# Kernel tuning notes

Hardware: AMD Instinct MI355X
Metric: run time of the kernel (lower is better)

Reference implementation:

```python
import jax, jax.numpy as jnp
import numpy as np

E = 256      # emb_size
H = 100      # ff_sim hidden
B, TQ, TK = 16, 128, 128


def setup_inputs() -> dict:
    key = jax.random.key(0)
    ks = jax.random.split(key, 8)
    queries = jax.random.normal(ks[0], (B, TQ, E), dtype=jnp.float32)
    keys = jax.random.normal(ks[1], (B, TK, E), dtype=jnp.float32)
    query_masks = jnp.ones((B, TQ), dtype=jnp.float32)
    key_masks = jnp.ones((B, TK), dtype=jnp.float32)
    # xavier_uniform bounds: sqrt(6/(fan_in+fan_out))
    def xavier(k, shape):
        fan_out, fan_in = shape
        lim = np.sqrt(6.0 / (fan_in + fan_out))
        return jax.random.uniform(k, shape, jnp.float32, -lim, lim)
    W1 = xavier(ks[2], (H, 2 * E))          # linear_ff_sim[0].weight
    b1 = jnp.zeros((H,), dtype=jnp.float32)  # linear_ff_sim[0].bias
    W2 = xavier(ks[3], (1, H))              # linear_ff_sim[2].weight (no bias)
    Wlast = xavier(ks[4], (E, 2 * E))       # linear_last.weight
    blast = jnp.zeros((E,), dtype=jnp.float32)
    return {"queries": queries, "keys": keys, "query_masks": query_masks,
            "key_masks": key_masks, "W1": W1, "b1": b1, "W2": W2,
            "Wlast": Wlast, "blast": blast}


def reference(queries, keys, query_masks, key_masks, W1, b1, W2, Wlast, blast):
    # forward calls attention_fc(keys, queries, key_masks, query_masks):
    #   attn queries = keys,  attn keys = queries,
    #   attn query_masks = key_masks, attn key_masks = query_masks.
    e = queries.shape[-1]
    # Additive-attention MLP score, decomposed: cat([keys_i, queries_j]) @ W1^T
    #   = keys_i @ W1[:, :E]^T + queries_j @ W1[:, E:]^T
    a = jnp.einsum('bie,he->bih', keys, W1[:, :e])      # [B,Tk,H]
    c = jnp.einsum('bje,he->bjh', queries, W1[:, e:])   # [B,Tq,H]
    h = jnp.tanh(a[:, :, None, :] + c[:, None, :, :] + b1)  # [B,Tk,Tq,H]
    sim = jnp.einsum('bijh,h->bij', h, W2[0])           # [B,Tk,Tq]
    neg = jnp.asarray(-2.0 ** 32 + 1, sim.dtype)
    sim = jnp.where(query_masks[:, None, :] == 0, neg, sim)
    sim = jax.nn.softmax(sim, axis=-1)
    sim = sim * key_masks[:, :, None]
    keys_attn = jnp.einsum('bij,bje->bie', sim, queries)  # [B,Tk,E]
    feature_mul = keys_attn * keys
    d = keys_attn - keys
    feature_sub = d * d
    feature_last = jnp.concatenate([feature_mul, feature_sub], axis=-1)  # [B,Tk,2E]
    return jax.nn.relu(jnp.einsum('bif,ef->bie', feature_last, Wlast) + blast)
```

## Files before the change

kernel.cpp:

```cpp
#include <hip/hip_runtime.h>


namespace {
constexpr int B  = 16;
constexpr int TQ = 128;
constexpr int TK = 128;
constexpr int E  = 256;
constexpr int H  = 100;
constexpr int HP = 112;
constexpr int G  = 4;
}

typedef __attribute__((ext_vector_type(8))) short short8;
typedef __attribute__((ext_vector_type(4))) float f32x4;

__device__ __forceinline__ unsigned short f2bf(float f) {
  unsigned u = __builtin_bit_cast(unsigned, f);
  u = (u + 0x7FFFu + ((u >> 16) & 1u)) >> 16;
  return (unsigned short)u;
}

__global__ __launch_bounds__(256) void convert_bf16(
    const float* __restrict__ queries, const float* __restrict__ keys,
    const float* __restrict__ W1, const float* __restrict__ Wlast,
    unsigned short* __restrict__ Xb, unsigned short* __restrict__ Wb1,
    unsigned short* __restrict__ Wb) {
  const int blk = blockIdx.x, t = threadIdx.x;
  if (blk < 1024) {
    const int idx = blk * 1024 + t * 4;
    const int row = idx >> 8, e = idx & 255;
    const float* src = (row < B * TK) ? keys + (size_t)row * E + e
                                      : queries + (size_t)(row - B * TK) * E + e;
    float4 v = *(const float4*)src;
    ushort4 o = make_ushort4(f2bf(v.x), f2bf(v.y), f2bf(v.z), f2bf(v.w));
    *(ushort4*)(Xb + idx) = o;
  } else if (blk < 1080) {
    const int idx = (blk - 1024) * 1024 + t * 4;
    const int h = idx >> 9;
    float4 v = (h < H) ? *(const float4*)(W1 + idx)
                       : make_float4(0.f, 0.f, 0.f, 0.f);
    ushort4 o = make_ushort4(f2bf(v.x), f2bf(v.y), f2bf(v.z), f2bf(v.w));
    *(ushort4*)(Wb1 + idx) = o;
  } else {
    const int idx = (blk - 1080) * 1024 + t * 4;
    float4 v = *(const float4*)(Wlast + idx);
    ushort4 o = make_ushort4(f2bf(v.x), f2bf(v.y), f2bf(v.z), f2bf(v.w));
    *(ushort4*)(Wb + idx) = o;
  }
}

__global__ __launch_bounds__(256) void prep_mfma(
    const unsigned short* __restrict__ Xb, const unsigned short* __restrict__ Wb1,
    const float* __restrict__ b1, float* __restrict__ A, float* __restrict__ C) {
  __shared__ short Bs[112 * 264];
  __shared__ short As[16 * 264];
  const int t  = threadIdx.x;
  const int m0 = blockIdx.x * 16;
  const bool isA = (m0 < B * TK);
  const int koff = isA ? 0 : 256;
  float* dst = isA ? (A + (size_t)m0 * HP)
                   : (C + (size_t)(m0 - B * TK) * HP);

  #pragma unroll
  for (int i = 0; i < 14; ++i) {
    const int idx = i * 256 + t;
    const int h = idx >> 5, seg = idx & 31;
    *(uint4*)(Bs + h * 264 + seg * 8) =
        *(const uint4*)(Wb1 + (size_t)h * 512 + koff + seg * 8);
  }
  #pragma unroll
  for (int i = 0; i < 2; ++i) {
    const int idx = i * 256 + t;
    const int r = idx >> 5, seg = idx & 31;
    *(uint4*)(As + r * 264 + seg * 8) =
        *(const uint4*)(Xb + (size_t)(m0 + r) * 256 + seg * 8);
  }
  __syncthreads();

  const int wave = t >> 6, lane = t & 63;
  const int m = lane & 15, kq = lane >> 4;
  const int nt0 = wave, nt1 = wave + 4;
  f32x4 acc0 = {0.f, 0.f, 0.f, 0.f}, acc1 = {0.f, 0.f, 0.f, 0.f};

  #pragma unroll
  for (int kc = 0; kc < 8; ++kc) {
    short8 a = *(const short8*)(As + m * 264 + kc * 32 + kq * 8);
    short8 bv0 = *(const short8*)(Bs + (nt0 * 16 + m) * 264 + kc * 32 + kq * 8);
    acc0 = __builtin_amdgcn_mfma_f32_16x16x32_bf16(a, bv0, acc0, 0, 0, 0);
    if (nt1 < 7) {
      short8 bv1 = *(const short8*)(Bs + (nt1 * 16 + m) * 264 + kc * 32 + kq * 8);
      acc1 = __builtin_amdgcn_mfma_f32_16x16x32_bf16(a, bv1, acc1, 0, 0, 0);
    }
  }

  const int rbase = (lane >> 4) * 4;
  {
    const int h = nt0 * 16 + m;
    const float bias = (isA && h < H) ? b1[h] : 0.0f;
    #pragma unroll
    for (int r = 0; r < 4; ++r)
      dst[(size_t)(rbase + r) * HP + h] = acc0[r] + bias;
  }
  if (nt1 < 7) {
    const int h = nt1 * 16 + m;
    const float bias = (isA && h < H) ? b1[h] : 0.0f;
    #pragma unroll
    for (int r = 0; r < 4; ++r)
      dst[(size_t)(rbase + r) * HP + h] = acc1[r] + bias;
  }
}

__global__ __launch_bounds__(512) void attn_core(
    const float* __restrict__ queries, const float* __restrict__ keys,
    const float* __restrict__ qmask, const float* __restrict__ kmask,
    const float* __restrict__ W2, const float* __restrict__ A,
    const float* __restrict__ C, unsigned short* __restrict__ feat ) {
  __shared__ float a_s[G * HP];
  __shared__ float w2s[HP];
  __shared__ float qm[TQ];
  __shared__ float simP[G * 512];
  __shared__ float pL[G * TQ];
  __shared__ float red[8];

  const int t   = threadIdx.x;
  const int blk = blockIdx.x;
  const int b   = blk >> 5;
  const int i0  = (blk & 31) * G;

  if (t < G * HP / 4)
    ((float4*)a_s)[t] = ((const float4*)(A + ((size_t)b * TK + i0) * HP))[t];
  if (t < HP) w2s[t] = (t < H) ? W2[t] : 0.0f;
  if (t < TQ) qm[t]  = qmask[b * TQ + t];
  __syncthreads();

  const int j = t & (TQ - 1);
  const int q = t >> 7;
  float4 cr[7], wr[7];
  float wsum = 0.0f;
  {
    const float4* c4 = (const float4*)(C + ((size_t)b * TQ + j) * HP + q * 28);
    const float4* w4 = (const float4*)w2s + q * 7;
    #pragma unroll
    for (int k = 0; k < 7; ++k) {
      cr[k] = c4[k];
      wr[k] = w4[k];
      wsum += wr[k].x + wr[k].y + wr[k].z + wr[k].w;
    }
  }
  {
    const float4* a4p = (const float4*)a_s + q * 7;
    #pragma unroll
    for (int g = 0; g < G; ++g) {
      float s = 0.0f;
      #pragma unroll
      for (int k = 0; k < 7; ++k) {
        float4 a4 = a4p[g * (HP / 4) + k];
        float x0 = a4.x + cr[k].x, x1 = a4.y + cr[k].y;
        float x2 = a4.z + cr[k].z, x3 = a4.w + cr[k].w;
        s = fmaf(wr[k].x, __builtin_amdgcn_rcpf(__expf(x0 + x0) + 1.0f), s);
        s = fmaf(wr[k].y, __builtin_amdgcn_rcpf(__expf(x1 + x1) + 1.0f), s);
        s = fmaf(wr[k].z, __builtin_amdgcn_rcpf(__expf(x2 + x2) + 1.0f), s);
        s = fmaf(wr[k].w, __builtin_amdgcn_rcpf(__expf(x3 + x3) + 1.0f), s);
      }
      simP[g * 512 + t] = wsum - 2.0f * s;
    }
  }
  __syncthreads();

  {
    const int g2 = t >> 7, j2 = t & 127;
    const float* sp = simP + g2 * 512 + j2;
    float sv = sp[0] + sp[128] + sp[256] + sp[384];
    if (qm[j2] == 0.0f) sv = -4294967295.0f;
    float p = __expf(sv);
    float s = p;
    #pragma unroll
    for (int off = 1; off < 64; off <<= 1) s += __shfl_xor(s, off, 64);
    if ((t & 63) == 0) red[t >> 6] = s;
    __syncthreads();
    pL[t] = p / (red[g2 * 2] + red[g2 * 2 + 1]);
  }
  __syncthreads();

  {
    const int e = t & 255, gh = t >> 8;
    float ka0 = 0.0f, ka1 = 0.0f;
    const float* qb = queries + (size_t)b * TQ * E + e;
    const float4* p4 = (const float4*)pL;
    for (int j4 = 0; j4 < TQ / 4; ++j4) {
      float4 p0 = p4[(gh * 2) * 32 + j4];
      float4 p1 = p4[(gh * 2 + 1) * 32 + j4];
      #pragma unroll
      for (int c = 0; c < 4; ++c) {
        float qv = qb[(size_t)(j4 * 4 + c) * E];
        ka0 = fmaf(((const float*)&p0)[c], qv, ka0);
        ka1 = fmaf(((const float*)&p1)[c], qv, ka1);
      }
    }
    #pragma unroll
    for (int gg = 0; gg < 2; ++gg) {
      const int g = gh * 2 + gg;
      const float ka = gg ? ka1 : ka0;
      const float kmv = kmask[b * TK + i0 + g];
      const float kav = ka * kmv;
      const float kv  = keys[((size_t)b * TK + i0 + g) * E + e];
      const size_t row = (size_t)(b * TK + i0 + g) * (2 * E);
      feat[row + e]     = f2bf(kav * kv);
      float d = kav - kv;
      feat[row + E + e] = f2bf(d * d);
    }
  }
}

__global__ __launch_bounds__(256) void last_gemm(
    const unsigned short* __restrict__ Wb ,
    const float* __restrict__ blast, float* __restrict__ out) {
  __shared__ short A_s[16 * 520];
  __shared__ short B_s[256 * 72];
  const int t  = threadIdx.x;
  const int m0 = blockIdx.x * 16;

  {
    const uint4* src = (const uint4*)out;
    #pragma unroll
    for (int i = 0; i < 4; ++i) {
      int idx = t + i * 256;
      int r = idx >> 6, c = idx & 63;
      *(uint4*)(A_s + r * 520 + c * 8) = src[(size_t)(m0 + r) * 64 + c];
    }
  }
  __syncthreads();

  f32x4 acc[4];
  #pragma unroll
  for (int nt = 0; nt < 4; ++nt) acc[nt] = f32x4{0.f, 0.f, 0.f, 0.f};

  const int wave = t >> 6, lane = t & 63;
  const int nsub = wave * 64;
  const int m    = lane & 15, kq = lane >> 4;

  for (int kc = 0; kc < 8; ++kc) {
    #pragma unroll
    for (int i = 0; i < 8; ++i) {
      int idx = t + i * 256;
      int r = idx >> 3, p = idx & 7;
      *(uint4*)(B_s + r * 72 + p * 8) =
          ((const uint4*)(Wb + (size_t)r * 512 + kc * 64))[p];
    }
    __syncthreads();
    #pragma unroll
    for (int ks = 0; ks < 2; ++ks) {
      short8 a = *(const short8*)(A_s + m * 520 + kc * 64 + ks * 32 + kq * 8);
      #pragma unroll
      for (int nt = 0; nt < 4; ++nt) {
        short8 bf = *(const short8*)(B_s + (nsub + nt * 16 + m) * 72 + ks * 32 + kq * 8);
        acc[nt] = __builtin_amdgcn_mfma_f32_16x16x32_bf16(a, bf, acc[nt], 0, 0, 0);
      }
    }
    __syncthreads();
  }

  const int col = lane & 15;
  const int rbase = m0 + (lane >> 4) * 4;
  #pragma unroll
  for (int nt = 0; nt < 4; ++nt) {
    const int e = nsub + nt * 16 + col;
    const float bl = blast[e];
    #pragma unroll
    for (int r = 0; r < 4; ++r)
      out[(size_t)(rbase + r) * 256 + e] = fmaxf(acc[nt][r] + bl, 0.0f);
  }
}

extern "C" void kernel_launch(void* const* d_in, const int* in_sizes, int n_in,
                              void* d_out, int out_size, void* d_ws, size_t ws_size,
                              hipStream_t stream) {
  (void)in_sizes; (void)n_in; (void)out_size; (void)ws_size;
  const float* queries = (const float*)d_in[0];
  const float* keys    = (const float*)d_in[1];
  const float* qmask   = (const float*)d_in[2];
  const float* kmask   = (const float*)d_in[3];
  const float* W1      = (const float*)d_in[4];
  const float* b1      = (const float*)d_in[5];
  const float* W2      = (const float*)d_in[6];
  const float* Wlast   = (const float*)d_in[7];
  const float* blast   = (const float*)d_in[8];
  float* out = (float*)d_out;

  float* A = (float*)d_ws;
  float* C = A + (size_t)B * TK * HP;
  unsigned short* Wb  = (unsigned short*)(C + (size_t)B * TQ * HP);
  unsigned short* Wb1 = Wb + (size_t)256 * 512;
  unsigned short* Xb  = Wb1 + (size_t)112 * 512;

  convert_bf16<<<dim3(1208), dim3(256), 0, stream>>>(
      queries, keys, W1, Wlast, Xb, Wb1, Wb);
  prep_mfma<<<dim3(256), dim3(256), 0, stream>>>(Xb, Wb1, b1, A, C);
  attn_core<<<dim3(B * (TK / G)), dim3(512), 0, stream>>>(
      queries, keys, qmask, kmask, W2, A, C, (unsigned short*)out);
  last_gemm<<<dim3(B * TK / 16), dim3(256), 0, stream>>>(Wb, blast, out);
}
```

Before: 99.08 us.

## Fuse bf16 conversion into prep and last GEMM into attention kernel

New measurement: 100.4 us. About the same (+1.3%).

```diff
diff --git a/kernel.cpp b/kernel.cpp
--- a/kernel.cpp
+++ b/kernel.cpp
@@ -8,7 +8,8 @@
 constexpr int E  = 256;
 constexpr int H  = 100;
 constexpr int HP = 112;
-constexpr int G  = 4;
+constexpr int G  = 8;
+constexpr float SC = 2.8853900817779268f;
 }
 
 typedef __attribute__((ext_vector_type(8))) short short8;
@@ -19,39 +20,16 @@
   u = (u + 0x7FFFu + ((u >> 16) & 1u)) >> 16;
   return (unsigned short)u;
 }
-
-__global__ __launch_bounds__(256) void convert_bf16(
+__device__ __forceinline__ unsigned pk2(float x, float y) {
+  return (unsigned)f2bf(x) | ((unsigned)f2bf(y) << 16);
+}
+
+__global__ __launch_bounds__(256) void prep_mfma(
     const float* __restrict__ queries, const float* __restrict__ keys,
-    const float* __restrict__ W1, const float* __restrict__ Wlast,
-    unsigned short* __restrict__ Xb, unsigned short* __restrict__ Wb1,
+    const float* __restrict__ W1, const float* __restrict__ b1,
+    const float* __restrict__ Wlast,
+    float* __restrict__ A, float* __restrict__ C,
     unsigned short* __restrict__ Wb) {
-  const int blk = blockIdx.x, t = threadIdx.x;
-  if (blk < 1024) {
-    const int idx = blk * 1024 + t * 4;
-    const int row = idx >> 8, e = idx & 255;
-    const float* src = (row < B * TK) ? keys + (size_t)row * E + e
-                                      : queries + (size_t)(row - B * TK) * E + e;
-    float4 v = *(const float4*)src;
-    ushort4 o = make_ushort4(f2bf(v.x), f2bf(v.y), f2bf(v.z), f2bf(v.w));
-    *(ushort4*)(Xb + idx) = o;
-  } else if (blk < 1080) {
-    const int idx = (blk - 1024) * 1024 + t * 4;
-    const int h = idx >> 9;
-    float4 v = (h < H) ? *(const float4*)(W1 + idx)
-                       : make_float4(0.f, 0.f, 0.f, 0.f);
-    ushort4 o = make_ushort4(f2bf(v.x), f2bf(v.y), f2bf(v.z), f2bf(v.w));
-    *(ushort4*)(Wb1 + idx) = o;
-  } else {
-    const int idx = (blk - 1080) * 1024 + t * 4;
-    float4 v = *(const float4*)(Wlast + idx);
-    ushort4 o = make_ushort4(f2bf(v.x), f2bf(v.y), f2bf(v.z), f2bf(v.w));
-    *(ushort4*)(Wb + idx) = o;
-  }
-}
-
-__global__ __launch_bounds__(256) void prep_mfma(
-    const unsigned short* __restrict__ Xb, const unsigned short* __restrict__ Wb1,
-    const float* __restrict__ b1, float* __restrict__ A, float* __restrict__ C) {
   __shared__ short Bs[112 * 264];
   __shared__ short As[16 * 264];
   const int t  = threadIdx.x;
@@ -61,19 +39,33 @@
   float* dst = isA ? (A + (size_t)m0 * HP)
                    : (C + (size_t)(m0 - B * TK) * HP);
 
+  {
+    const int base = blockIdx.x * 512 + t * 2;
+    float2 w = *(const float2*)(Wlast + base);
+    *(unsigned*)(Wb + base) = pk2(w.x, w.y);
+  }
   #pragma unroll
   for (int i = 0; i < 14; ++i) {
     const int idx = i * 256 + t;
     const int h = idx >> 5, seg = idx & 31;
-    *(uint4*)(Bs + h * 264 + seg * 8) =
-        *(const uint4*)(Wb1 + (size_t)h * 512 + koff + seg * 8);
+    uint4 o = make_uint4(0u, 0u, 0u, 0u);
+    if (h < H) {
+      const float4* p = (const float4*)(W1 + (size_t)h * 512 + koff + seg * 8);
+      float4 u = p[0], v = p[1];
+      o = make_uint4(pk2(u.x, u.y), pk2(u.z, u.w), pk2(v.x, v.y), pk2(v.z, v.w));
+    }
+    *(uint4*)(Bs + h * 264 + seg * 8) = o;
   }
   #pragma unroll
   for (int i = 0; i < 2; ++i) {
     const int idx = i * 256 + t;
     const int r = idx >> 5, seg = idx & 31;
+    const float* src = isA ? (keys + (size_t)(m0 + r) * E)
+                           : (queries + (size_t)(m0 - B * TK + r) * E);
+    const float4* p = (const float4*)(src + seg * 8);
+    float4 u = p[0], v = p[1];
     *(uint4*)(As + r * 264 + seg * 8) =
-        *(const uint4*)(Xb + (size_t)(m0 + r) * 256 + seg * 8);
+        make_uint4(pk2(u.x, u.y), pk2(u.z, u.w), pk2(v.x, v.y), pk2(v.z, v.w));
   }
   __syncthreads();
 
@@ -99,38 +91,44 @@
     const float bias = (isA && h < H) ? b1[h] : 0.0f;
     #pragma unroll
     for (int r = 0; r < 4; ++r)
-      dst[(size_t)(rbase + r) * HP + h] = acc0[r] + bias;
+      dst[(size_t)(rbase + r) * HP + h] = (acc0[r] + bias) * SC;
   }
   if (nt1 < 7) {
     const int h = nt1 * 16 + m;
     const float bias = (isA && h < H) ? b1[h] : 0.0f;
     #pragma unroll
     for (int r = 0; r < 4; ++r)
-      dst[(size_t)(rbase + r) * HP + h] = acc1[r] + bias;
-  }
-}
-
-__global__ __launch_bounds__(512) void attn_core(
+      dst[(size_t)(rbase + r) * HP + h] = (acc1[r] + bias) * SC;
+  }
+}
+
+__global__ __launch_bounds__(512) void attn_gemm(
     const float* __restrict__ queries, const float* __restrict__ keys,
     const float* __restrict__ qmask, const float* __restrict__ kmask,
-    const float* __restrict__ W2, const float* __restrict__ A,
-    const float* __restrict__ C, unsigned short* __restrict__ feat ) {
+    const float* __restrict__ W2, const float* __restrict__ blast,
+    const float* __restrict__ A, const float* __restrict__ C,
+    const unsigned short* __restrict__ Wb, float* __restrict__ out) {
   __shared__ float a_s[G * HP];
   __shared__ float w2s[HP];
   __shared__ float qm[TQ];
   __shared__ float simP[G * 512];
   __shared__ float pL[G * TQ];
-  __shared__ float red[8];
+  __shared__ short featL[16 * 520];
 
   const int t   = threadIdx.x;
   const int blk = blockIdx.x;
-  const int b   = blk >> 5;
-  const int i0  = (blk & 31) * G;
+  const int b   = blk >> 4;
+  const int i0  = (blk & 15) * G;
 
   if (t < G * HP / 4)
     ((float4*)a_s)[t] = ((const float4*)(A + ((size_t)b * TK + i0) * HP))[t];
   if (t < HP) w2s[t] = (t < H) ? W2[t] : 0.0f;
   if (t < TQ) qm[t]  = qmask[b * TQ + t];
+  #pragma unroll
+  for (int i = 0; i < 2; ++i) {
+    int idx = t + i * 512;
+    if (idx < 520) ((uint4*)(featL + 8 * 520))[idx] = make_uint4(0u, 0u, 0u, 0u);
+  }
   __syncthreads();
 
   const int j = t & (TQ - 1);
@@ -154,13 +152,11 @@
       float s = 0.0f;
       #pragma unroll
       for (int k = 0; k < 7; ++k) {
-        float4 a4 = a4p[g * (HP / 4) + k];
-        float x0 = a4.x + cr[k].x, x1 = a4.y + cr[k].y;
-        float x2 = a4.z + cr[k].z, x3 = a4.w + cr[k].w;
-        s = fmaf(wr[k].x, __builtin_amdgcn_rcpf(__expf(x0 + x0) + 1.0f), s);
-        s = fmaf(wr[k].y, __builtin_amdgcn_rcpf(__expf(x1 + x1) + 1.0f), s);
-        s = fmaf(wr[k].z, __builtin_amdgcn_rcpf(__expf(x2 + x2) + 1.0f), s);
-        s = fmaf(wr[k].w, __builtin_amdgcn_rcpf(__expf(x3 + x3) + 1.0f), s);
+        float4 a4 = a4p[g * 28 + k];
+        s = fmaf(wr[k].x, __builtin_amdgcn_rcpf(exp2f(a4.x + cr[k].x) + 1.0f), s);
+        s = fmaf(wr[k].y, __builtin_amdgcn_rcpf(exp2f(a4.y + cr[k].y) + 1.0f), s);
+        s = fmaf(wr[k].z, __builtin_amdgcn_rcpf(exp2f(a4.z + cr[k].z) + 1.0f), s);
+        s = fmaf(wr[k].w, __builtin_amdgcn_rcpf(exp2f(a4.w + cr[k].w) + 1.0f), s);
       }
       simP[g * 512 + t] = wsum - 2.0f * s;
     }
@@ -168,107 +164,78 @@
   __syncthreads();
 
   {
-    const int g2 = t >> 7, j2 = t & 127;
-    const float* sp = simP + g2 * 512 + j2;
-    float sv = sp[0] + sp[128] + sp[256] + sp[384];
-    if (qm[j2] == 0.0f) sv = -4294967295.0f;
-    float p = __expf(sv);
-    float s = p;
+    const int g = t >> 6, lane = t & 63;
+    const float* sp = simP + g * 512;
+    float sv0 = sp[lane]      + sp[128 + lane]      + sp[256 + lane]      + sp[384 + lane];
+    float sv1 = sp[lane + 64] + sp[128 + lane + 64] + sp[256 + lane + 64] + sp[384 + lane + 64];
+    if (qm[lane] == 0.0f)      sv0 = -4294967295.0f;
+    if (qm[lane + 64] == 0.0f) sv1 = -4294967295.0f;
+    float p0 = __expf(sv0), p1 = __expf(sv1);
+    float s = p0 + p1;
     #pragma unroll
     for (int off = 1; off < 64; off <<= 1) s += __shfl_xor(s, off, 64);
-    if ((t & 63) == 0) red[t >> 6] = s;
-    __syncthreads();
-    pL[t] = p / (red[g2 * 2] + red[g2 * 2 + 1]);
+    float inv = __builtin_amdgcn_rcpf(s);
+    pL[g * TQ + lane]      = p0 * inv;
+    pL[g * TQ + lane + 64] = p1 * inv;
   }
   __syncthreads();
 
   {
     const int e = t & 255, gh = t >> 8;
-    float ka0 = 0.0f, ka1 = 0.0f;
+    float ka[4] = {0.f, 0.f, 0.f, 0.f};
     const float* qb = queries + (size_t)b * TQ * E + e;
-    const float4* p4 = (const float4*)pL;
+    const float4* p4 = (const float4*)pL + (gh * 4) * 32;
     for (int j4 = 0; j4 < TQ / 4; ++j4) {
-      float4 p0 = p4[(gh * 2) * 32 + j4];
-      float4 p1 = p4[(gh * 2 + 1) * 32 + j4];
+      float4 pv[4];
+      #pragma unroll
+      for (int gg = 0; gg < 4; ++gg) pv[gg] = p4[gg * 32 + j4];
       #pragma unroll
       for (int c = 0; c < 4; ++c) {
         float qv = qb[(size_t)(j4 * 4 + c) * E];
-        ka0 = fmaf(((const float*)&p0)[c], qv, ka0);
-        ka1 = fmaf(((const float*)&p1)[c], qv, ka1);
-      }
-    }
-    #pragma unroll
-    for (int gg = 0; gg < 2; ++gg) {
-      const int g = gh * 2 + gg;
-      const float ka = gg ? ka1 : ka0;
+        #pragma unroll
+        for (int gg = 0; gg < 4; ++gg)
+          ka[gg] = fmaf(((const float*)&pv[gg])[c], qv, ka[gg]);
+      }
+    }
+    #pragma unroll
+    for (int gg = 0; gg < 4; ++gg) {
+      const int g = gh * 4 + gg;
       const float kmv = kmask[b * TK + i0 + g];
-      const float kav = ka * kmv;
+      const float kav = ka[gg] * kmv;
       const float kv  = keys[((size_t)b * TK + i0 + g) * E + e];
-      const size_t row = (size_t)(b * TK + i0 + g) * (2 * E);
-      feat[row + e]     = f2bf(kav * kv);
+      featL[g * 520 + e]     = (short)f2bf(kav * kv);
       float d = kav - kv;
-      feat[row + E + e] = f2bf(d * d);
-    }
-  }
-}
-
-__global__ __launch_bounds__(256) void last_gemm(
-    const unsigned short* __restrict__ Wb ,
-    const float* __restrict__ blast, float* __restrict__ out) {
-  __shared__ short A_s[16 * 520];
-  __shared__ short B_s[256 * 72];
-  const int t  = threadIdx.x;
-  const int m0 = blockIdx.x * 16;
-
-  {
-    const uint4* src = (const uint4*)out;
-    #pragma unroll
-    for (int i = 0; i < 4; ++i) {
-      int idx = t + i * 256;
-      int r = idx >> 6, c = idx & 63;
-      *(uint4*)(A_s + r * 520 + c * 8) = src[(size_t)(m0 + r) * 64 + c];
-    }
-  }
-  __syncthreads();
-
-  f32x4 acc[4];
-  #pragma unroll
-  for (int nt = 0; nt < 4; ++nt) acc[nt] = f32x4{0.f, 0.f, 0.f, 0.f};
-
-  const int wave = t >> 6, lane = t & 63;
-  const int nsub = wave * 64;
-  const int m    = lane & 15, kq = lane >> 4;
-
-  for (int kc = 0; kc < 8; ++kc) {
-    #pragma unroll
-    for (int i = 0; i < 8; ++i) {
-      int idx = t + i * 256;
-      int r = idx >> 3, p = idx & 7;
-      *(uint4*)(B_s + r * 72 + p * 8) =
-          ((const uint4*)(Wb + (size_t)r * 512 + kc * 64))[p];
-    }
-    __syncthreads();
-    #pragma unroll
-    for (int ks = 0; ks < 2; ++ks) {
-      short8 a = *(const short8*)(A_s + m * 520 + kc * 64 + ks * 32 + kq * 8);
-      #pragma unroll
-      for (int nt = 0; nt < 4; ++nt) {
-        short8 bf = *(const short8*)(B_s + (nsub + nt * 16 + m) * 72 + ks * 32 + kq * 8);
+      featL[g * 520 + E + e] = (short)f2bf(d * d);
+    }
+  }
+  __syncthreads();
+
+  {
+    const int wave = t >> 6, lane = t & 63;
+    const int m = lane & 15, kq = lane >> 4;
+    f32x4 acc[2] = {{0.f, 0.f, 0.f, 0.f}, {0.f, 0.f, 0.f, 0.f}};
+    #pragma unroll
+    for (int kc = 0; kc < 16; ++kc) {
+      short8 a = *(const short8*)(featL + m * 520 + kc * 32 + kq * 8);
+      #pragma unroll
+      for (int nt = 0; nt < 2; ++nt) {
+        const int ncol = wave * 32 + nt * 16 + m;
+        short8 bf = *(const short8*)(Wb + (size_t)ncol * 512 + kc * 32 + kq * 8);
         acc[nt] = __builtin_amdgcn_mfma_f32_16x16x32_bf16(a, bf, acc[nt], 0, 0, 0);
       }
     }
-    __syncthreads();
-  }
-
-  const int col = lane & 15;
-  const int rbase = m0 + (lane >> 4) * 4;
-  #pragma unroll
-  for (int nt = 0; nt < 4; ++nt) {
-    const int e = nsub + nt * 16 + col;
-    const float bl = blast[e];
-    #pragma unroll
-    for (int r = 0; r < 4; ++r)
-      out[(size_t)(rbase + r) * 256 + e] = fmaxf(acc[nt][r] + bl, 0.0f);
+    const int rbase = (lane >> 4) * 4;
+    if (rbase < 8) {
+      #pragma unroll
+      for (int nt = 0; nt < 2; ++nt) {
+        const int ncol = wave * 32 + nt * 16 + (lane & 15);
+        const float bl = blast[ncol];
+        #pragma unroll
+        for (int r = 0; r < 4; ++r)
+          out[((size_t)b * TK + i0 + rbase + r) * E + ncol] =
+              fmaxf(acc[nt][r] + bl, 0.0f);
+      }
+    }
   }
 }
 
@@ -289,14 +256,10 @@
 
   float* A = (float*)d_ws;
   float* C = A + (size_t)B * TK * HP;
-  unsigned short* Wb  = (unsigned short*)(C + (size_t)B * TQ * HP);
-  unsigned short* Wb1 = Wb + (size_t)256 * 512;
-  unsigned short* Xb  = Wb1 + (size_t)112 * 512;
-
-  convert_bf16<<<dim3(1208), dim3(256), 0, stream>>>(
-      queries, keys, W1, Wlast, Xb, Wb1, Wb);
-  prep_mfma<<<dim3(256), dim3(256), 0, stream>>>(Xb, Wb1, b1, A, C);
-  attn_core<<<dim3(B * (TK / G)), dim3(512), 0, stream>>>(
-      queries, keys, qmask, kmask, W2, A, C, (unsigned short*)out);
-  last_gemm<<<dim3(B * TK / 16), dim3(256), 0, stream>>>(Wb, blast, out);
-}
+  unsigned short* Wb = (unsigned short*)(C + (size_t)B * TQ * HP);
+
+  prep_mfma<<<dim3(256), dim3(256), 0, stream>>>(
+      queries, keys, W1, b1, Wlast, A, C, Wb);
+  attn_gemm<<<dim3(B * (TK / G)), dim3(512), 0, stream>>>(
+      queries, keys, qmask, kmask, W2, blast, A, C, Wb, out);
+}
```
